# Optimization experiments

Measured on AMD Instinct MI355X. Metric: run time of the kernel, lower is better.

Reference implementation:

```python
import jax, jax.numpy as jnp
import numpy as np

N = 50000       # num nodes
E = 600000      # num edges
IN = 128        # in_channels
H = 4           # heads
C = 32          # out_channels per head
B = 3           # num bends (Bezier control points)
NEG_SLOPE = 0.2


def setup_inputs() -> dict:
    key = jax.random.key(0)
    ks = jax.random.split(key, 6)
    x = jax.random.normal(ks[0], (N, IN), dtype=jnp.float32)
    edge_index = jax.random.randint(ks[1], (2, E), 0, N)
    # Bezier coefficients at t=0.5 for a 3-point curve: [0.25, 0.5, 0.25]
    coeffs_t = jnp.array([0.25, 0.5, 0.25], dtype=jnp.float32)
    glorot_w = float(np.sqrt(2.0) * np.sqrt(6.0 / (H * C + IN)))
    glorot_a = float(np.sqrt(2.0) * np.sqrt(6.0 / (1 + C)))
    lin_weight = jax.random.uniform(ks[2], (B, H * C, IN), jnp.float32, -glorot_w, glorot_w)
    lin_bias = jnp.zeros((B, H * C), dtype=jnp.float32)
    att_src = jax.random.uniform(ks[3], (B, 1, H, C), jnp.float32, -glorot_a, glorot_a)
    att_dst = jax.random.uniform(ks[4], (B, 1, H, C), jnp.float32, -glorot_a, glorot_a)
    return {"x": x, "edge_index": edge_index, "coeffs_t": coeffs_t,
            "lin_weight": lin_weight, "lin_bias": lin_bias,
            "att_src": att_src, "att_dst": att_dst}


def reference(x, edge_index, coeffs_t, lin_weight, lin_bias, att_src, att_dst):
    # Bezier parameter interpolation: weighted sum over bends
    W = jnp.einsum('b,boi->oi', coeffs_t, lin_weight)      # [H*C, IN]
    bias = jnp.einsum('b,bo->o', coeffs_t, lin_bias)       # [H*C]
    a_src = jnp.einsum('b,bqhc->qhc', coeffs_t, att_src)   # [1,H,C]
    a_dst = jnp.einsum('b,bqhc->qhc', coeffs_t, att_dst)   # [1,H,C]

    n = x.shape[0]
    xt = (x @ W.T + bias).reshape(n, H, C)                 # [N,H,C]
    alpha_src = jnp.sum(xt * a_src, axis=-1)               # [N,H]
    alpha_dst = jnp.sum(xt * a_dst, axis=-1)               # [N,H]

    row, col = edge_index[0], edge_index[1]
    alpha = alpha_src[row] + alpha_dst[col]                # [E,H]
    alpha = jax.nn.leaky_relu(alpha, NEG_SLOPE)

    # scatter-softmax over incoming edges of each target node (col)
    amax = jax.ops.segment_max(alpha, col, num_segments=n)  # [N,H]
    ex = jnp.exp(alpha - amax[col])                         # [E,H]
    denom = jax.ops.segment_sum(ex, col, num_segments=n)    # [N,H]
    alpha = ex / (denom[col] + 1e-16)                       # [E,H]

    # weighted neighbor aggregation (edge-parallel segment reduction)
    msg = xt[row] * alpha[..., None]                        # [E,H,C]
    out = jax.ops.segment_sum(msg, col, num_segments=n)     # [N,H,C]
    return out.reshape(n, H * C)                            # concat=True
```

## Files before the change

### kernel.cpp

```cpp
#include <hip/hip_runtime.h>
#include <hip/hip_bf16.h>

#define GAT_IN   128
#define GAT_OUT  128
#define GAT_H    4
#define GAT_C    32
#define NEG_SLOPE 0.2f
#define BUCKET   48
#define NBF      1563
#define NBPAD    1568
#define CAPF     640
#define E_B      2048
#define EPTH     8

typedef __attribute__((ext_vector_type(8))) short bf16x8;
typedef __attribute__((ext_vector_type(4))) float f32x4;
union U4 { uint4 u; bf16x8 v; };

static __device__ __forceinline__ unsigned int pack_bf16(float lo, float hi) {
    __hip_bfloat16 a = __float2bfloat16(lo);
    __hip_bfloat16 b = __float2bfloat16(hi);
    unsigned short ua = *reinterpret_cast<unsigned short*>(&a);
    unsigned short ub = *reinterpret_cast<unsigned short*>(&b);
    return (unsigned int)ua | ((unsigned int)ub << 16);
}

__global__ __launch_bounds__(256) void interp_kernel(
    const float* __restrict__ coeffs,
    const float* __restrict__ lw,
    const float* __restrict__ lb,
    const float* __restrict__ asr,
    const float* __restrict__ ads,
    unsigned int* __restrict__ wfrag,
    float* __restrict__ biasc,
    float* __restrict__ asrc, float* __restrict__ adst,
    int* __restrict__ bucket_pos)
{
    int b = blockIdx.x, t = threadIdx.x;
    int i = b * 256 + t;
    float c0 = coeffs[0], c1 = coeffs[1], c2 = coeffs[2];
    int lane = (i >> 2) & 63;
    int nk   = i >> 8;
    int jw   = i & 3;
    int nt = nk >> 2, ks = nk & 3;
    int o = nt * 16 + (lane & 15);
    int k = ks * 32 + (lane >> 4) * 8 + jw * 2;
    int idx = o * 128 + k;
    float w0 = c0 * lw[idx]     + c1 * lw[16384 + idx]     + c2 * lw[32768 + idx];
    float w1 = c0 * lw[idx + 1] + c1 * lw[16384 + idx + 1] + c2 * lw[32768 + idx + 1];
    wfrag[i] = pack_bf16(w0, w1);
    if (b == 0) {
        if (t < 128) {
            biasc[t] = c0 * lb[t]  + c1 * lb[128 + t]  + c2 * lb[256 + t];
            asrc[t]  = c0 * asr[t] + c1 * asr[128 + t] + c2 * asr[256 + t];
            adst[t]  = c0 * ads[t] + c1 * ads[128 + t] + c2 * ads[256 + t];
        }
        for (int j = t; j < NBPAD; j += 256) bucket_pos[j] = 0;
    }
}

static __device__ __forceinline__ void pass1_body(
    int blk, int* hist, int* hist2, int* gbase,
    const int* __restrict__ ei, int ne,
    int* __restrict__ bucket_pos,
    unsigned int* __restrict__ coarse)
{
    int tid = threadIdx.x;
    int b0  = blk * E_B;

    for (int i = tid; i < NBPAD; i += 256) { hist[i] = 0; hist2[i] = 0; }

    int rows[EPTH], cols[EPTH];
    #pragma unroll
    for (int i = 0; i < EPTH; ++i) {
        int e = b0 + i * 256 + tid;
        cols[i] = (e < ne) ? ei[ne + e] : -1;
    }
    #pragma unroll
    for (int i = 0; i < EPTH; ++i) {
        int e = b0 + i * 256 + tid;
        rows[i] = (e < ne) ? ei[e] : 0;
    }
    __syncthreads();

    #pragma unroll
    for (int i = 0; i < EPTH; ++i)
        if (cols[i] >= 0) atomicAdd(&hist[cols[i] >> 5], 1);
    __syncthreads();

    for (int i = tid; i < NBPAD; i += 256)
        gbase[i] = hist[i] ? atomicAdd(&bucket_pos[i], hist[i]) : 0;
    __syncthreads();

    #pragma unroll
    for (int i = 0; i < EPTH; ++i) {
        if (cols[i] >= 0) {
            int bk  = cols[i] >> 5;
            int pos = gbase[bk] + atomicAdd(&hist2[bk], 1);
            if (pos < CAPF)
                coarse[bk * CAPF + pos] =
                    ((unsigned int)cols[i] << 16) | (unsigned int)rows[i];
        }
    }
}

static __device__ __forceinline__ void gemm_body(
    int bu, float* C,
    const float* __restrict__ x,
    const unsigned int* __restrict__ wfrag,
    const float* __restrict__ biasc,
    const float* __restrict__ asrc,
    const float* __restrict__ adst,
    unsigned int* __restrict__ xtb,
    float* __restrict__ alpha_src,
    float* __restrict__ alpha_dst,
    int n)
{
    int tid  = threadIdx.x;
    int lane = tid & 63;
    int wave = tid >> 6;
    int quad = lane >> 4;
    int lm   = lane & 15;
    int m0   = bu * 64 + wave * 16;

    uint4* wl = (uint4*)C;
    const uint4* wf = (const uint4*)wfrag;
    #pragma unroll
    for (int i = 0; i < 8; ++i)
        wl[tid + i * 256] = wf[tid + i * 256];

    int arow = m0 + lm; if (arow >= n) arow = n - 1;
    const float4* xr = (const float4*)(x + (size_t)arow * 128 + quad * 8);
    float4 a[8];
    #pragma unroll
    for (int ks = 0; ks < 4; ++ks) {
        a[2 * ks]     = xr[ks * 8 + 0];
        a[2 * ks + 1] = xr[ks * 8 + 1];
    }

    f32x4 acc[8];
    #pragma unroll
    for (int t = 0; t < 8; ++t) acc[t] = (f32x4){0.f, 0.f, 0.f, 0.f};

    __syncthreads();

    #pragma unroll
    for (int ks = 0; ks < 4; ++ks) {
        U4 af;
        af.u.x = pack_bf16(a[2*ks].x, a[2*ks].y);
        af.u.y = pack_bf16(a[2*ks].z, a[2*ks].w);
        af.u.z = pack_bf16(a[2*ks+1].x, a[2*ks+1].y);
        af.u.w = pack_bf16(a[2*ks+1].z, a[2*ks+1].w);
        #pragma unroll
        for (int nt = 0; nt < 8; ++nt) {
            U4 bf; bf.u = wl[(nt * 4 + ks) * 64 + lane];
            acc[nt] = __builtin_amdgcn_mfma_f32_16x16x32_bf16(
                af.v, bf.v, acc[nt], 0, 0, 0);
        }
    }
    __syncthreads();

    #pragma unroll
    for (int nt = 0; nt < 8; ++nt) {
        int col = nt * 16 + lm;
        #pragma unroll
        for (int r = 0; r < 4; ++r) {
            int rowl = wave * 16 + quad * 4 + r;
            C[rowl * 132 + col] = acc[nt][r];
        }
    }
    __syncthreads();

    int rowl = wave * 16 + (lane >> 2);
    int seg  = lane & 3;
    int mrow = bu * 64 + rowl;
    if (mrow < n) {
        const float4* cb = (const float4*)(C + rowl * 132 + seg * 32);
        const float4* bb = (const float4*)(biasc + seg * 32);
        const float4* sb = (const float4*)(asrc + seg * 32);
        const float4* db = (const float4*)(adst + seg * 32);
        float s = 0.f, d = 0.f;
        unsigned int ow[16];
        #pragma unroll
        for (int q = 0; q < 8; ++q) {
            float4 v = cb[q];
            float4 b = bb[q];
            v.x += b.x; v.y += b.y; v.z += b.z; v.w += b.w;
            float4 as = sb[q], ad = db[q];
            s += v.x * as.x + v.y * as.y + v.z * as.z + v.w * as.w;
            d += v.x * ad.x + v.y * ad.y + v.z * ad.z + v.w * ad.w;
            ow[q * 2 + 0] = pack_bf16(v.x, v.y);
            ow[q * 2 + 1] = pack_bf16(v.z, v.w);
        }
        alpha_src[mrow * 4 + seg] = s;
        alpha_dst[mrow * 4 + seg] = d;
        uint4* xo = (uint4*)(xtb + (size_t)mrow * 64 + seg * 16);
        #pragma unroll
        for (int q4 = 0; q4 < 4; ++q4)
            xo[q4] = make_uint4(ow[q4 * 4], ow[q4 * 4 + 1],
                                ow[q4 * 4 + 2], ow[q4 * 4 + 3]);
    }
}

__global__ __launch_bounds__(256) void fused_p1_gemm_kernel(
    const int* __restrict__ ei, int ne,
    int* __restrict__ bucket_pos,
    unsigned int* __restrict__ coarse,
    const float* __restrict__ x,
    const unsigned int* __restrict__ wfrag,
    const float* __restrict__ biasc,
    const float* __restrict__ asrc,
    const float* __restrict__ adst,
    unsigned int* __restrict__ xtb,
    float* __restrict__ alpha_src,
    float* __restrict__ alpha_dst,
    int n, int p1b)
{
    __shared__ __align__(16) unsigned char smem[64 * 132 * 4];
    int b = blockIdx.x;
    if (b < p1b) {
        int* hist  = (int*)smem;
        int* hist2 = hist + NBPAD;
        int* gbase = hist2 + NBPAD;
        pass1_body(b, hist, hist2, gbase, ei, ne, bucket_pos, coarse);
    } else {
        gemm_body(b - p1b, (float*)smem, x, wfrag, biasc, asrc, adst,
                  xtb, alpha_src, alpha_dst, n);
    }
}

static __device__ __forceinline__ void window16(
    uint4 qa, uint4 qb, int rem,
    unsigned int h, unsigned int sl, float ad,
    const unsigned int* __restrict__ xtb,
    const float* __restrict__ alpha_src,
    float& den, float4& acc)
{
    unsigned int w[8] = {qa.x, qa.y, qa.z, qa.w, qb.x, qb.y, qb.z, qb.w};
    int r[16];
    #pragma unroll
    for (int t = 0; t < 16; ++t) {
        unsigned int rr = (t & 1) ? (w[t >> 1] >> 16) : (w[t >> 1] & 0xFFFFu);
        r[t] = (t < rem) ? (int)rr : 0;
    }

    float as[16];
    #pragma unroll
    for (int t = 0; t < 16; ++t)
        as[t] = alpha_src[(((unsigned)r[t]) << 2) | h];
    uint2 u[16];
    #pragma unroll
    for (int t = 0; t < 16; ++t)
        u[t] = *(const uint2*)(xtb + ((((unsigned)r[t]) << 6) + (sl << 1)));

    float e[16];
    #pragma unroll
    for (int t = 0; t < 16; ++t) {
        float a = as[t] + ad;
        a = fmaxf(a, NEG_SLOPE * a);
        float ex = __expf(a);
        e[t] = (t < rem) ? ex : 0.f;
    }
    float s01 = e[0]+e[1],   s23 = e[2]+e[3],   s45 = e[4]+e[5],   s67 = e[6]+e[7];
    float s89 = e[8]+e[9],   sab = e[10]+e[11], scd = e[12]+e[13], sef = e[14]+e[15];
    den += ((s01+s23) + (s45+s67)) + ((s89+sab) + (scd+sef));

    #pragma unroll
    for (int t = 0; t < 16; ++t) {
        acc.x = fmaf(e[t], __uint_as_float(u[t].x << 16),          acc.x);
        acc.y = fmaf(e[t], __uint_as_float(u[t].x & 0xFFFF0000u),  acc.y);
        acc.z = fmaf(e[t], __uint_as_float(u[t].y << 16),          acc.z);
        acc.w = fmaf(e[t], __uint_as_float(u[t].y & 0xFFFF0000u),  acc.w);
    }
}

__global__ __launch_bounds__(256) void pass2agg_kernel(
    const int* __restrict__ bucket_pos,
    const unsigned int* __restrict__ coarse,
    const unsigned int* __restrict__ xtb,
    const float* __restrict__ alpha_src,
    const float* __restrict__ alpha_dst,
    float* __restrict__ out,
    int n)
{
    __shared__ __align__(16) unsigned short st[32 * BUCKET];
    __shared__ int lcnt[32];
    int b = blockIdx.x;
    int tid = threadIdx.x;
    if (tid < 32) lcnt[tid] = 0;
    __syncthreads();

    int cb = bucket_pos[b]; if (cb > CAPF) cb = CAPF;
    const unsigned int* cp = coarse + (size_t)b * CAPF;
    for (int i = tid; i < cb; i += 256) {
        unsigned int v = cp[i];
        int lc = (int)(v >> 16) & 31;
        int pos = atomicAdd(&lcnt[lc], 1);
        if (pos < BUCKET)
            st[lc * BUCKET + pos] = (unsigned short)(v & 0xFFFFu);
    }
    __syncthreads();

    int wave = tid >> 6;
    unsigned int lane = tid & 63;
    unsigned int subn = lane >> 5;
    unsigned int sl  = lane & 31;
    unsigned int h   = sl >> 3;
    int nbase = b * 32;

    #pragma unroll
    for (int pass = 0; pass < 4; ++pass) {
        int ln = pass * 8 + wave * 2 + (int)subn;
        int node = nbase + ln;
        bool active = node < n;
        int nodec = active ? node : 0;
        int m = lcnt[ln]; if (!active) m = 0; if (m > BUCKET) m = BUCKET;
        float ad = alpha_dst[((unsigned)nodec << 2) | h];
        const uint4* sq = (const uint4*)(st + ln * BUCKET);
        uint4 qa = sq[0];
        uint4 qb = sq[1];

        float4 acc = make_float4(0.f, 0.f, 0.f, 0.f);
        float den = 0.f;
        window16(qa, qb, m, h, sl, ad, xtb, alpha_src, den, acc);
        for (int j = 16; j < m; j += 16) {
            int q = j >> 3;
            window16(sq[q], sq[q + 1], m - j, h, sl, ad, xtb, alpha_src,
                     den, acc);
        }
        if (active) {
            float inv = 1.0f / (den + 1e-16f);
            ((float4*)out)[((unsigned)node << 5) | sl] =
                make_float4(acc.x * inv, acc.y * inv, acc.z * inv,
                            acc.w * inv);
        }
    }
}

extern "C" void kernel_launch(void* const* d_in, const int* in_sizes, int n_in,
                              void* d_out, int out_size, void* d_ws, size_t ws_size,
                              hipStream_t stream)
{
    const float* x      = (const float*)d_in[0];
    const int*   ei     = (const int*)  d_in[1];
    const float* coeffs = (const float*)d_in[2];
    const float* lw     = (const float*)d_in[3];
    const float* lb     = (const float*)d_in[4];
    const float* asr    = (const float*)d_in[5];
    const float* ads    = (const float*)d_in[6];
    float* out = (float*)d_out;

    int n  = in_sizes[0] / GAT_IN;
    int ne = in_sizes[1] / 2;

    float* ws        = (float*)d_ws;
    unsigned int* wfrag = (unsigned int*)ws;
    float* biasc     = ws + 16384;
    float* asrc      = ws + 16512;
    float* adst      = ws + 16640;
    unsigned int* xtb = (unsigned int*)(ws + 16768);
    float* alpha_src = (float*)(xtb + (size_t)n * 64);
    float* alpha_dst = alpha_src + (size_t)n * 4;
    int*   bucket_pos = (int*)(alpha_dst + (size_t)n * 4);
    unsigned int* coarse = (unsigned int*)(bucket_pos + 2048);

    int p1b = (ne + E_B - 1) / E_B;
    int gu  = (n + 63) / 64;

    interp_kernel<<<32, 256, 0, stream>>>(
        coeffs, lw, lb, asr, ads, wfrag, biasc, asrc, adst, bucket_pos);
    fused_p1_gemm_kernel<<<p1b + gu, 256, 0, stream>>>(
        ei, ne, bucket_pos, coarse,
        x, wfrag, biasc, asrc, adst, xtb, alpha_src, alpha_dst, n, p1b);
    pass2agg_kernel<<<NBF, 256, 0, stream>>>(
        bucket_pos, coarse, xtb, alpha_src, alpha_dst, out, n);
}
```

Before: 142.3 us.

## Split aggregation by head with XCC-affine persistent work-stealing blocks

Replaces the per-bucket aggregation grid with a persistent kernel. Blocks pull bucket indices from one atomic counter per head. Each block starts on the head matching its XCC id, so each XCC's L2 mainly caches one head's 64-byte slice of the bf16 feature rows, and each thread now loads 4 bytes per neighbor instead of 8. The cost is that each bucket's edge list is re-read and re-sorted into shared memory once per head, and dynamic scheduling adds atomics and extra barriers.

New measurement: 284.6 us. 2x slower.

```diff
diff --git a/kernel.cpp b/kernel.cpp
--- a/kernel.cpp
+++ b/kernel.cpp
@@ -55,7 +55,7 @@
             asrc[t]  = c0 * asr[t] + c1 * asr[128 + t] + c2 * asr[256 + t];
             adst[t]  = c0 * ads[t] + c1 * ads[128 + t] + c2 * ads[256 + t];
         }
-        for (int j = t; j < NBPAD; j += 256) bucket_pos[j] = 0;
+        for (int j = t; j < 2048; j += 256) bucket_pos[j] = 0;
     }
 }
 
@@ -229,12 +229,12 @@
     }
 }
 
-static __device__ __forceinline__ void window16(
+static __device__ __forceinline__ void window16h(
     uint4 qa, uint4 qb, int rem,
-    unsigned int h, unsigned int sl, float ad,
+    unsigned int h, unsigned int sl16, float ad,
     const unsigned int* __restrict__ xtb,
     const float* __restrict__ alpha_src,
-    float& den, float4& acc)
+    float& den, float& ax, float& ay)
 {
     unsigned int w[8] = {qa.x, qa.y, qa.z, qa.w, qb.x, qb.y, qb.z, qb.w};
     int r[16];
@@ -248,10 +248,10 @@
     #pragma unroll
     for (int t = 0; t < 16; ++t)
         as[t] = alpha_src[(((unsigned)r[t]) << 2) | h];
-    uint2 u[16];
+    unsigned int u[16];
     #pragma unroll
     for (int t = 0; t < 16; ++t)
-        u[t] = *(const uint2*)(xtb + ((((unsigned)r[t]) << 6) + (sl << 1)));
+        u[t] = xtb[(((unsigned)r[t]) << 6) + (h << 4) + sl16];
 
     float e[16];
     #pragma unroll
@@ -267,72 +267,78 @@
 
     #pragma unroll
     for (int t = 0; t < 16; ++t) {
-        acc.x = fmaf(e[t], __uint_as_float(u[t].x << 16),          acc.x);
-        acc.y = fmaf(e[t], __uint_as_float(u[t].x & 0xFFFF0000u),  acc.y);
-        acc.z = fmaf(e[t], __uint_as_float(u[t].y << 16),          acc.z);
-        acc.w = fmaf(e[t], __uint_as_float(u[t].y & 0xFFFF0000u),  acc.w);
-    }
-}
-
-__global__ __launch_bounds__(256) void pass2agg_kernel(
+        ax = fmaf(e[t], __uint_as_float(u[t] << 16),          ax);
+        ay = fmaf(e[t], __uint_as_float(u[t] & 0xFFFF0000u),  ay);
+    }
+}
+
+__global__ __launch_bounds__(256) void p2agg_kernel(
     const int* __restrict__ bucket_pos,
     const unsigned int* __restrict__ coarse,
     const unsigned int* __restrict__ xtb,
     const float* __restrict__ alpha_src,
     const float* __restrict__ alpha_dst,
+    int* __restrict__ prog,
     float* __restrict__ out,
     int n)
 {
     __shared__ __align__(16) unsigned short st[32 * BUCKET];
     __shared__ int lcnt[32];
-    int b = blockIdx.x;
+    __shared__ int s_b;
     int tid = threadIdx.x;
-    if (tid < 32) lcnt[tid] = 0;
-    __syncthreads();
-
-    int cb = bucket_pos[b]; if (cb > CAPF) cb = CAPF;
-    const unsigned int* cp = coarse + (size_t)b * CAPF;
-    for (int i = tid; i < cb; i += 256) {
-        unsigned int v = cp[i];
-        int lc = (int)(v >> 16) & 31;
-        int pos = atomicAdd(&lcnt[lc], 1);
-        if (pos < BUCKET)
-            st[lc * BUCKET + pos] = (unsigned short)(v & 0xFFFFu);
-    }
-    __syncthreads();
-
-    int wave = tid >> 6;
-    unsigned int lane = tid & 63;
-    unsigned int subn = lane >> 5;
-    unsigned int sl  = lane & 31;
-    unsigned int h   = sl >> 3;
-    int nbase = b * 32;
-
-    #pragma unroll
-    for (int pass = 0; pass < 4; ++pass) {
-        int ln = pass * 8 + wave * 2 + (int)subn;
-        int node = nbase + ln;
-        bool active = node < n;
-        int nodec = active ? node : 0;
-        int m = lcnt[ln]; if (!active) m = 0; if (m > BUCKET) m = BUCKET;
-        float ad = alpha_dst[((unsigned)nodec << 2) | h];
-        const uint4* sq = (const uint4*)(st + ln * BUCKET);
-        uint4 qa = sq[0];
-        uint4 qb = sq[1];
-
-        float4 acc = make_float4(0.f, 0.f, 0.f, 0.f);
-        float den = 0.f;
-        window16(qa, qb, m, h, sl, ad, xtb, alpha_src, den, acc);
-        for (int j = 16; j < m; j += 16) {
-            int q = j >> 3;
-            window16(sq[q], sq[q + 1], m - j, h, sl, ad, xtb, alpha_src,
-                     den, acc);
-        }
-        if (active) {
-            float inv = 1.0f / (den + 1e-16f);
-            ((float4*)out)[((unsigned)node << 5) | sl] =
-                make_float4(acc.x * inv, acc.y * inv, acc.z * inv,
-                            acc.w * inv);
+
+    unsigned int xcc;
+    asm volatile("s_getreg_b32 %0, hwreg(HW_REG_XCC_ID)" : "=s"(xcc));
+    int h0 = (int)(xcc & 3);
+
+    for (int hp = 0; hp < 4; ++hp) {
+        unsigned int h = (unsigned int)((h0 + hp) & 3);
+        while (true) {
+            __syncthreads();
+            if (tid == 0) s_b = atomicAdd(&prog[h], 1);
+            __syncthreads();
+            int b = s_b;
+            if (b >= NBF) break;
+
+            if (tid < 32) lcnt[tid] = 0;
+            __syncthreads();
+            int cb = bucket_pos[b]; if (cb > CAPF) cb = CAPF;
+            const unsigned int* cp = coarse + (size_t)b * CAPF;
+            for (int i = tid; i < cb; i += 256) {
+                unsigned int v = cp[i];
+                int lc = (int)(v >> 16) & 31;
+                int pos = atomicAdd(&lcnt[lc], 1);
+                if (pos < BUCKET)
+                    st[lc * BUCKET + pos] = (unsigned short)(v & 0xFFFFu);
+            }
+            __syncthreads();
+
+            unsigned int sl16 = tid & 15;
+            #pragma unroll
+            for (int pass = 0; pass < 2; ++pass) {
+                int ln = pass * 16 + (tid >> 4);
+                int node = b * 32 + ln;
+                bool active = node < n;
+                int nodec = active ? node : 0;
+                int m = lcnt[ln]; if (!active) m = 0; if (m > BUCKET) m = BUCKET;
+                float ad = alpha_dst[((unsigned)nodec << 2) | h];
+                const uint4* sq = (const uint4*)(st + ln * BUCKET);
+                uint4 qa = sq[0];
+                uint4 qb = sq[1];
+
+                float ax = 0.f, ay = 0.f, den = 0.f;
+                window16h(qa, qb, m, h, sl16, ad, xtb, alpha_src, den, ax, ay);
+                for (int j = 16; j < m; j += 16) {
+                    int q = j >> 3;
+                    window16h(sq[q], sq[q + 1], m - j, h, sl16, ad,
+                              xtb, alpha_src, den, ax, ay);
+                }
+                if (active) {
+                    float inv = 1.0f / (den + 1e-16f);
+                    ((float2*)out)[((unsigned)node << 6) | (h << 4) | sl16] =
+                        make_float2(ax * inv, ay * inv);
+                }
+            }
         }
     }
 }
@@ -362,6 +368,7 @@
     float* alpha_src = (float*)(xtb + (size_t)n * 64);
     float* alpha_dst = alpha_src + (size_t)n * 4;
     int*   bucket_pos = (int*)(alpha_dst + (size_t)n * 4);
+    int*   prog       = bucket_pos + 1600;
     unsigned int* coarse = (unsigned int*)(bucket_pos + 2048);
 
     int p1b = (ne + E_B - 1) / E_B;
@@ -372,6 +379,6 @@
     fused_p1_gemm_kernel<<<p1b + gu, 256, 0, stream>>>(
         ei, ne, bucket_pos, coarse,
         x, wfrag, biasc, asrc, adst, xtb, alpha_src, alpha_dst, n, p1b);
-    pass2agg_kernel<<<NBF, 256, 0, stream>>>(
-        bucket_pos, coarse, xtb, alpha_src, alpha_dst, out, n);
-}
+    p2agg_kernel<<<2048, 256, 0, stream>>>(
+        bucket_pos, coarse, xtb, alpha_src, alpha_dst, prog, out, n);
+}
```
